# Kernel optimization log

Hardware: AMD Instinct MI355X
Metric: run time of the kernel (lower is better)

The kernel has to match this reference:

```python
import jax, jax.numpy as jnp
import numpy as np

EMBED_DIM = 1024
N_HEADS = 16
HEAD_DIM = EMBED_DIM // N_HEADS


def setup_inputs() -> dict:
    key = jax.random.key(0)
    k1, k2, k3 = jax.random.split(key, 3)
    B, T, C = 2, 2048, EMBED_DIM
    x = jax.random.normal(k1, (B, T, C), dtype=jnp.float32)
    # nn.Linear-style init scale
    s = 1.0 / np.sqrt(C)
    Wqkv = jax.random.normal(k2, (C, 3 * C), dtype=jnp.float32) * s
    bqkv = jnp.zeros((3 * C,), dtype=jnp.float32)
    Wout = jax.random.normal(k3, (C, C), dtype=jnp.float32) * s
    bout = jnp.zeros((C,), dtype=jnp.float32)
    return {"x": x, "Wqkv": Wqkv, "bqkv": bqkv, "Wout": Wout, "bout": bout}


def reference(x, Wqkv, bqkv, Wout, bout):
    B, T, C = x.shape
    H, D = N_HEADS, HEAD_DIM
    qkv = x @ Wqkv + bqkv  # [B,T,3C]
    q, k, v = jnp.split(qkv, 3, axis=-1)
    # [B,T,C] -> [B,H,T,D]
    q = q.reshape(B, T, H, D).transpose(0, 2, 1, 3)
    k = k.reshape(B, T, H, D).transpose(0, 2, 1, 3)
    v = v.reshape(B, T, H, D).transpose(0, 2, 1, 3)
    scale = 1.0 / np.sqrt(D)
    scores = jnp.einsum("bhqd,bhkd->bhqk", q, k) * scale  # [B,H,T,T]
    causal = jnp.tril(jnp.ones((T, T), dtype=bool))  # True where allowed
    scores = jnp.where(causal, scores, jnp.finfo(scores.dtype).min)
    attn = jax.nn.softmax(scores, axis=-1)
    out = jnp.einsum("bhqk,bhkd->bhqd", attn, v)  # [B,H,T,D]
    out = out.transpose(0, 2, 1, 3).reshape(B, T, C)
    return out @ Wout + bout
```

## Files before the change

### kernel.cpp

```cpp
#include <hip/hip_runtime.h>
#include <hip/hip_bf16.h>
#include <stdint.h>

#define EMBED 1024
#define NH 16
#define HD 64
#define BATCH 2
#define SEQ 2048
#define MTOK (BATCH*SEQ)

using bf8 = __attribute__((ext_vector_type(8))) short;
using f4  = __attribute__((ext_vector_type(4))) float;
using f16v = __attribute__((ext_vector_type(16))) float;
using u16x4 = __attribute__((ext_vector_type(4))) unsigned short;

union U4 { uint32_t u[4]; bf8 v; };

__device__ __forceinline__ uint32_t pk_bf16(float a, float b) {
  __hip_bfloat162 h = __float22bfloat162_rn(float2{a, b});
  union { __hip_bfloat162 h; uint32_t u; } c; c.h = h; return c.u;
}
__device__ __forceinline__ unsigned short bfbits(float f) {
  __hip_bfloat16 h = __float2bfloat16(f);
  union { __hip_bfloat16 h; unsigned short u; } c; c.h = h; return c.u;
}
__device__ __forceinline__ float bf2f(unsigned short u) {
  union { uint32_t u; float f; } c; c.u = (uint32_t)u << 16; return c.f;
}
__device__ __forceinline__ float fexp2(float x) {
#if __has_builtin(__builtin_amdgcn_exp2f)
  return __builtin_amdgcn_exp2f(x);
#else
  return exp2f(x);
#endif
}
__device__ __forceinline__ float frcp(float x) {
#if __has_builtin(__builtin_amdgcn_rcpf)
  return __builtin_amdgcn_rcpf(x);
#else
  return 1.f / x;
#endif
}

__device__ __forceinline__ void gl2lds16(const void* g, void* l) {
  __builtin_amdgcn_global_load_lds(
      (const __attribute__((address_space(1))) void*)g,
      (__attribute__((address_space(3))) void*)l, 16, 0, 0);
}

__global__ __launch_bounds__(256) void prep(const float* __restrict__ x,
                                            unsigned short* __restrict__ xb,
                                            const float* __restrict__ Wqkv,
                                            unsigned short* __restrict__ wqkvT,
                                            const float* __restrict__ Wout,
                                            unsigned short* __restrict__ woutT) {
  __shared__ float tl[64][65];
  int blk = blockIdx.x;
  if (blk < 4096) {
    int i = (blk * 256 + threadIdx.x) * 4;
    float4 v = *(const float4*)(x + i);
    uint2 o;
    o.x = pk_bf16(v.x, v.y);
    o.y = pk_bf16(v.z, v.w);
    *(uint2*)(xb + i) = o;
    return;
  }
  const float* W; unsigned short* Wt; int K, N, bx, by;
  if (blk < 4096 + 768) {
    int j = blk - 4096; W = Wqkv; Wt = wqkvT; K = 1024; N = 3072;
    bx = j % 48; by = j / 48;
  } else {
    int j = blk - 4096 - 768; W = Wout; Wt = woutT; K = 1024; N = 1024;
    bx = j % 16; by = j / 16;
  }
  int k0 = by * 64, n0 = bx * 64;
  int tr = threadIdx.x >> 6, tc = threadIdx.x & 63;
#pragma unroll
  for (int i = 0; i < 16; i++) {
    int r = tr + i * 4;
    tl[r][tc] = W[(size_t)(k0 + r) * N + n0 + tc];
  }
  __syncthreads();
#pragma unroll
  for (int i = 0; i < 16; i++) {
    int r = tr + i * 4;
    Wt[(size_t)(n0 + r) * K + k0 + tc] = bfbits(tl[tc][r]);
  }
}

template<int BN, int MODE>
__global__ __launch_bounds__(256) void gemm_bt(const unsigned short* __restrict__ A,
                                               const unsigned short* __restrict__ Bt,
                                               const float* __restrict__ bias,
                                               unsigned short* __restrict__ Oq,
                                               unsigned short* __restrict__ Ov,
                                               float* __restrict__ Of,
                                               int M, int N, int K) {
  constexpr int MT = (BN == 128) ? 4 : 2;
  const int tid = threadIdx.x;
  const int w = tid >> 6, lane = tid & 63;
  const int wm = (BN == 128) ? (w >> 1) : w;
  const int wn = (BN == 128) ? (w & 1) : 0;
  const int m0 = blockIdx.y * 128, n0 = blockIdx.x * BN;

  __shared__ char smem[16384 + BN * 128];
  char* Al = smem;
  char* Bl = smem + 16384;

  f4 acc[MT][4] = {};

  for (int k0 = 0; k0 < K; k0 += 64) {
    __syncthreads();
#pragma unroll
    for (int i = 0; i < 4; i++) {
      int row = w * 8 + i * 32 + (lane >> 3);
      int col = ((lane & 7) * 8) ^ ((row & 7) << 3);
      gl2lds16(A + (size_t)(m0 + row) * K + k0 + col, Al + (w * 8 + i * 32) * 128);
    }
#pragma unroll
    for (int i = 0; i < BN / 32; i++) {
      int row = w * 8 + i * 32 + (lane >> 3);
      int col = ((lane & 7) * 8) ^ ((row & 7) << 3);
      gl2lds16(Bt + (size_t)(n0 + row) * K + k0 + col, Bl + (w * 8 + i * 32) * 128);
    }
    __syncthreads();
#pragma unroll
    for (int ks = 0; ks < 2; ks++) {
      bf8 af[MT], bfr[4];
#pragma unroll
      for (int mt = 0; mt < MT; mt++) {
        int rr = wm * (MT * 16) + mt * 16 + (lane & 15);
        af[mt] = *(const bf8*)(Al + rr * 128 + ((ks * 64 + (lane >> 4) * 16) ^ ((rr & 7) << 4)));
      }
#pragma unroll
      for (int nt = 0; nt < 4; nt++) {
        int rr = wn * 64 + nt * 16 + (lane & 15);
        bfr[nt] = *(const bf8*)(Bl + rr * 128 + ((ks * 64 + (lane >> 4) * 16) ^ ((rr & 7) << 4)));
      }
#pragma unroll
      for (int mt = 0; mt < MT; mt++)
#pragma unroll
        for (int nt = 0; nt < 4; nt++)
          acc[mt][nt] = __builtin_amdgcn_mfma_f32_16x16x32_bf16(af[mt], bfr[nt], acc[mt][nt], 0, 0, 0);
    }
  }

  if (MODE == 0) {
#pragma unroll
    for (int nt = 0; nt < 4; nt++) {
      int n = n0 + wn * 64 + nt * 16 + (lane & 15);
      float bv = bias[n];
      int region = n >> 10, c = n & 1023, h = c >> 6, d = c & 63;
      float sc = (region == 0) ? 0.180336880f : 1.0f;
#pragma unroll
      for (int mt = 0; mt < MT; mt++) {
#pragma unroll
        for (int r = 0; r < 4; r++) {
          int m = m0 + wm * (MT * 16) + mt * 16 + (lane >> 4) * 4 + r;
          int b = m >> 11, t = m & 2047;
          unsigned short val = bfbits((acc[mt][nt][r] + bv) * sc);
          if (region < 2) {
            size_t off = ((((size_t)region * 2 + b) * 16 + h) * 2048 + t) * 64 + d;
            Oq[off] = val;
          } else {
            size_t off = (((size_t)b * 16 + h) * 64 + d) * 2048 + t;
            Ov[off] = val;
          }
        }
      }
    }
  } else {
#pragma unroll
    for (int mt = 0; mt < MT; mt++) {
#pragma unroll
      for (int r = 0; r < 4; r++) {
        int m = m0 + wm * (MT * 16) + mt * 16 + (lane >> 4) * 4 + r;
#pragma unroll
        for (int nt = 0; nt < 4; nt++) {
          int n = n0 + wn * 64 + nt * 16 + (lane & 15);
          Of[(size_t)m * N + n] = acc[mt][nt][r] + bias[n];
        }
      }
    }
  }
}

__global__ __launch_bounds__(256) void attn9(const unsigned short* __restrict__ Qb,
                                             const unsigned short* __restrict__ Kb,
                                             const unsigned short* __restrict__ Vtb,
                                             unsigned short* __restrict__ Ob,
                                             unsigned short* __restrict__ partO,
                                             float* __restrict__ Lbuf) {
  const int idx = blockIdx.x;
  int qt, ts, te;
  const int bh = idx & 31;
  if (idx < 256)        { qt = 8 + (idx >> 5);          ts = 0;  te = 16; }
  else if (idx < 512)   { qt = 8 + ((idx - 256) >> 5);  ts = 16; te = 2 * qt + 2; }
  else                  { qt = 7 - ((idx - 512) >> 5);  ts = 0;  te = 2 * qt + 2; }

  const int tid = threadIdx.x;
  const int w = tid >> 6, lane = tid & 63;
  const int hi = lane >> 5, q32 = lane & 31;

  __shared__ char smem[32768];

  const unsigned short* Qg  = Qb  + (size_t)bh * SEQ * HD;
  const unsigned short* Kg  = Kb  + (size_t)bh * SEQ * HD;
  const unsigned short* Vtg = Vtb + (size_t)bh * SEQ * HD;

  const int qbw  = qt * 128 + w * 32;
  const int qrow = qbw + q32;

  bf8 qf[4];
#pragma unroll
  for (int kc = 0; kc < 4; kc++)
    qf[kc] = *(const bf8*)(Qg + (size_t)qrow * HD + kc * 16 + hi * 8);

  U4 ones;
#pragma unroll
  for (int i = 0; i < 4; i++) ones.u[i] = 0x3F803F80u;

  f16v acc0 = {}, acc1 = {}, accl = {};

  auto STAGE = [&](int buf, int t) {
    int kv0 = t * 64;
#pragma unroll
    for (int i = 0; i < 2; i++) {
      int c = i * 4 + w;
      int row = c * 8 + (lane >> 3);
      int col = ((lane & 7) * 8) ^ ((row & 7) << 3);
      gl2lds16(Kg + (size_t)(kv0 + row) * HD + col,    smem + buf * 8192 + c * 1024);
      gl2lds16(Vtg + (size_t)row * SEQ + kv0 + col,    smem + 16384 + buf * 8192 + c * 1024);
    }
  };

  const int nt_loc = te - ts;
  STAGE(0, ts);
  if (nt_loc > 1) STAGE(1, ts + 1);

  for (int tl = 0; tl < nt_loc; tl++) {
    const int t = ts + tl;
    const int kv0 = t * 64;

    if (tl + 1 < nt_loc) {
      asm volatile("s_waitcnt vmcnt(4)" ::: "memory");
    } else {
      asm volatile("s_waitcnt vmcnt(0)" ::: "memory");
    }
    __builtin_amdgcn_s_barrier();

    if (kv0 <= qbw + 31) {
      const char* kl = smem + (tl & 1) * 8192;
      const char* vl = smem + 16384 + (tl & 1) * 8192;
      const bool hi_vis = (kv0 + 32 <= qbw + 31);

      f16v s0 = {}, s1 = {};
      __builtin_amdgcn_s_setprio(1);
#pragma unroll
      for (int kc = 0; kc < 4; kc++) {
        int r0 = q32;
        bf8 k0 = *(const bf8*)(kl + r0 * 128 + ((kc * 32 + hi * 16) ^ ((r0 & 7) << 4)));
        s0 = __builtin_amdgcn_mfma_f32_32x32x16_bf16(k0, qf[kc], s0, 0, 0, 0);
      }
      if (hi_vis) {
#pragma unroll
        for (int kc = 0; kc < 4; kc++) {
          int r1 = 32 + q32;
          bf8 k1 = *(const bf8*)(kl + r1 * 128 + ((kc * 32 + hi * 16) ^ ((r1 & 7) << 4)));
          s1 = __builtin_amdgcn_mfma_f32_32x32x16_bf16(k1, qf[kc], s1, 0, 0, 0);
        }
      }
      __builtin_amdgcn_s_setprio(0);

      if (kv0 + 63 > qbw) {
#pragma unroll
        for (int r = 0; r < 16; r++) {
          int key = kv0 + (r & 3) + 8 * (r >> 2) + 4 * hi;
          if (key > qrow)      s0[r] = -1e30f;
          if (key + 32 > qrow) s1[r] = -1e30f;
        }
      }

      uint32_t u[16];
#pragma unroll
      for (int m8 = 0; m8 < 8; m8++) {
        float pa = fexp2(s0[2 * m8]), pb = fexp2(s0[2 * m8 + 1]);
        u[m8] = pk_bf16(pa, pb);
      }
      if (hi_vis) {
#pragma unroll
        for (int m8 = 0; m8 < 8; m8++) {
          float pc = fexp2(s1[2 * m8]), pd = fexp2(s1[2 * m8 + 1]);
          u[8 + m8] = pk_bf16(pc, pd);
        }
      }

      __builtin_amdgcn_s_setprio(1);
      const int ncc = hi_vis ? 4 : 2;
      for (int kcc = 0; kcc < ncc; kcc++) {
        const int base = (kcc >> 1) * 8 + (kcc & 1) * 4;
        uint32_t a0 = u[base + 0], a2 = u[base + 2];
        uint32_t a1 = u[base + 1], a3 = u[base + 3];
        asm("v_permlane32_swap_b32 %0, %1" : "+v"(a0), "+v"(a2));
        asm("v_permlane32_swap_b32 %0, %1" : "+v"(a1), "+v"(a3));
        U4 f; f.u[0] = a0; f.u[1] = a1; f.u[2] = a2; f.u[3] = a3;
        int r0 = q32, r1 = 32 + q32;
        bf8 v0 = *(const bf8*)(vl + r0 * 128 + ((kcc * 32 + hi * 16) ^ ((r0 & 7) << 4)));
        bf8 v1 = *(const bf8*)(vl + r1 * 128 + ((kcc * 32 + hi * 16) ^ ((r1 & 7) << 4)));
        acc0 = __builtin_amdgcn_mfma_f32_32x32x16_bf16(f.v, v0, acc0, 0, 0, 0);
        acc1 = __builtin_amdgcn_mfma_f32_32x32x16_bf16(f.v, v1, acc1, 0, 0, 0);
        accl = __builtin_amdgcn_mfma_f32_32x32x16_bf16(f.v, ones.v, accl, 0, 0, 0);
      }
      __builtin_amdgcn_s_setprio(0);
    }

    __builtin_amdgcn_s_barrier();
    if (tl + 2 < nt_loc) STAGE(tl & 1, t + 2);
  }

  if (qt < 8) {
    int b = bh >> 4, h = bh & 15;
    unsigned short* Og = Ob + (size_t)b * SEQ * EMBED;
#pragma unroll
    for (int r = 0; r < 16; r++) {
      int ql_ = (r & 3) + 8 * (r >> 2) + 4 * hi;
      float linv = frcp(accl[r]);
      size_t rowoff = (size_t)(qbw + ql_) * EMBED + h * 64;
      Og[rowoff + q32]      = bfbits(acc0[r] * linv);
      Og[rowoff + 32 + q32] = bfbits(acc1[r] * linv);
    }
  } else {
    int seg = (ts == 16) ? 1 : 0;
    int part = ((qt - 8) * 32 + bh) * 2 + seg;
    unsigned short* P0 = partO + (size_t)part * 8192;
#pragma unroll
    for (int r = 0; r < 16; r++) {
      int ql_ = (r & 3) + 8 * (r >> 2) + 4 * hi;
      int rowl = w * 32 + ql_;
      P0[rowl * 64 + q32]      = bfbits(acc0[r]);
      P0[rowl * 64 + 32 + q32] = bfbits(acc1[r]);
    }
    if (q32 == 0) {
#pragma unroll
      for (int r = 0; r < 16; r++) {
        int ql_ = (r & 3) + 8 * (r >> 2) + 4 * hi;
        Lbuf[part * 128 + w * 32 + ql_] = accl[r];
      }
    }
  }
}

__global__ __launch_bounds__(256) void attn_combine(const unsigned short* __restrict__ partO,
                                                    const float* __restrict__ Lbuf,
                                                    unsigned short* __restrict__ Ob) {
  int pair = blockIdx.x;
  int qt = 8 + (pair >> 5), bh = pair & 31;
  int p0 = pair * 2, p1 = p0 + 1;
  int b = bh >> 4, h = bh & 15;
#pragma unroll
  for (int rr = 0; rr < 2; rr++) {
    int row = rr * 64 + (threadIdx.x >> 2);
    int d0 = (threadIdx.x & 3) * 16;
    float l0 = Lbuf[p0 * 128 + row], l1 = Lbuf[p1 * 128 + row];
    float linv = 1.f / (l0 + l1);
    const unsigned short* O0 = partO + (size_t)p0 * 8192 + row * 64 + d0;
    const unsigned short* O1 = partO + (size_t)p1 * 8192 + row * 64 + d0;
    unsigned short* out = Ob + ((size_t)b * SEQ + qt * 128 + row) * EMBED + h * 64 + d0;
    u16x4 res[4];
#pragma unroll
    for (int v = 0; v < 4; v++) {
      u16x4 a = *(const u16x4*)(O0 + v * 4);
      u16x4 c = *(const u16x4*)(O1 + v * 4);
#pragma unroll
      for (int e = 0; e < 4; e++)
        res[v][e] = bfbits(linv * (bf2f(a[e]) + bf2f(c[e])));
    }
    *(u16x4*)(out)      = res[0];
    *(u16x4*)(out + 4)  = res[1];
    *(u16x4*)(out + 8)  = res[2];
    *(u16x4*)(out + 12) = res[3];
  }
}

extern "C" void kernel_launch(void* const* d_in, const int* in_sizes, int n_in,
                              void* d_out, int out_size, void* d_ws, size_t ws_size,
                              hipStream_t stream) {
  const float* x    = (const float*)d_in[0];
  const float* Wqkv = (const float*)d_in[1];
  const float* bqkv = (const float*)d_in[2];
  const float* Wout = (const float*)d_in[3];
  const float* bout = (const float*)d_in[4];
  float* out = (float*)d_out;

  char* ws = (char*)d_ws;
  unsigned short* xb    = (unsigned short*)ws;
  unsigned short* partO = (unsigned short*)ws;
  unsigned short* wqkvT = (unsigned short*)(ws + (size_t)8  * 1048576);
  float*          lbuf  = (float*)(ws + (size_t)8 * 1048576);
  unsigned short* woutT = (unsigned short*)(ws + (size_t)14 * 1048576);
  unsigned short* qk    = (unsigned short*)(ws + (size_t)16 * 1048576);
  unsigned short* vT    = (unsigned short*)(ws + (size_t)32 * 1048576);
  unsigned short* obuf  = (unsigned short*)(ws + (size_t)40 * 1048576);

  prep<<<dim3(4096 + 768 + 256), 256, 0, stream>>>(x, xb, Wqkv, wqkvT, Wout, woutT);

  gemm_bt<128, 0><<<dim3(24, 32), 256, 0, stream>>>(xb, wqkvT, bqkv, qk, vT, nullptr,
                                                    MTOK, 3 * EMBED, EMBED);

  const unsigned short* Qb = qk;
  const unsigned short* Kb = qk + (size_t)BATCH * NH * SEQ * HD;
  attn9<<<dim3(768), 256, 0, stream>>>(Qb, Kb, vT, obuf, partO, lbuf);
  attn_combine<<<dim3(256), 256, 0, stream>>>(partO, lbuf, obuf);

  gemm_bt<64, 1><<<dim3(16, 32), 256, 0, stream>>>(obuf, woutT, bout, nullptr, nullptr, out,
                                                   MTOK, EMBED, EMBED);
}
```

Measured before the change: 114.3 us.

## Rebalance causal attention work with table-driven splits of at most eleven KV tiles

Replaces the fixed two-way KV split for the upper half of query tiles with a table-driven schedule. Every block now processes at most 11 KV tiles, long query tiles are split into two or three segments, and blocks are ordered longest first. The combine kernel handles a variable number of partials for query tiles 5 to 15. The aim is to reduce tail imbalance across the causal workload, at the cost of more blocks, more partial writes and a larger combine pass.

```diff
diff --git a/kernel.cpp b/kernel.cpp
--- a/kernel.cpp
+++ b/kernel.cpp
@@ -185,18 +185,21 @@
   }
 }
 
-__global__ __launch_bounds__(256) void attn9(const unsigned short* __restrict__ Qb,
-                                             const unsigned short* __restrict__ Kb,
-                                             const unsigned short* __restrict__ Vtb,
-                                             unsigned short* __restrict__ Ob,
-                                             unsigned short* __restrict__ partO,
-                                             float* __restrict__ Lbuf) {
+__global__ __launch_bounds__(256) void attn11(const unsigned short* __restrict__ Qb,
+                                              const unsigned short* __restrict__ Kb,
+                                              const unsigned short* __restrict__ Vtb,
+                                              unsigned short* __restrict__ Ob,
+                                              unsigned short* __restrict__ partO,
+                                              float* __restrict__ Lbuf) {
+  static const signed char QTs[32] = {15,15,14,14,13,13,12,12,11,11,10,10,9,8,7,6,5,15,4,9,14,3,8,13,2,7,12,1,6,11,0,5};
+  static const signed char TSs[32] = {0,11,0,11,0,11,0,11,0,11,0,11,0,0,0,0,0,22,0,11,22,0,11,22,0,11,22,0,11,22,0,11};
+  static const signed char PS[32]  = {0,1,2,3,4,5,6,7,8,9,10,11,12,13,14,15,16,17,-1,18,19,-1,20,21,-1,22,23,-1,24,25,-1,26};
   const int idx = blockIdx.x;
-  int qt, ts, te;
-  const int bh = idx & 31;
-  if (idx < 256)        { qt = 8 + (idx >> 5);          ts = 0;  te = 16; }
-  else if (idx < 512)   { qt = 8 + ((idx - 256) >> 5);  ts = 16; te = 2 * qt + 2; }
-  else                  { qt = 7 - ((idx - 512) >> 5);  ts = 0;  te = 2 * qt + 2; }
+  const int s = idx >> 5, bh = idx & 31;
+  const int qt = QTs[s], ts = TSs[s];
+  const int ntot = 2 * qt + 2;
+  const int te = min(ts + 11, ntot);
+  const int slot = PS[s];
 
   const int tid = threadIdx.x;
   const int w = tid >> 6, lane = tid & 63;
@@ -318,7 +321,7 @@
     if (tl + 2 < nt_loc) STAGE(tl & 1, t + 2);
   }
 
-  if (qt < 8) {
+  if (slot < 0) {
     int b = bh >> 4, h = bh & 15;
     unsigned short* Og = Ob + (size_t)b * SEQ * EMBED;
 #pragma unroll
@@ -330,9 +333,8 @@
       Og[rowoff + 32 + q32] = bfbits(acc1[r] * linv);
     }
   } else {
-    int seg = (ts == 16) ? 1 : 0;
-    int part = ((qt - 8) * 32 + bh) * 2 + seg;
-    unsigned short* P0 = partO + (size_t)part * 8192;
+    int pidx = slot * 32 + bh;
+    unsigned short* P0 = partO + (size_t)pidx * 8192;
 #pragma unroll
     for (int r = 0; r < 16; r++) {
       int ql_ = (r & 3) + 8 * (r >> 2) + 4 * hi;
@@ -344,7 +346,7 @@
 #pragma unroll
       for (int r = 0; r < 16; r++) {
         int ql_ = (r & 3) + 8 * (r >> 2) + 4 * hi;
-        Lbuf[part * 128 + w * 32 + ql_] = accl[r];
+        Lbuf[pidx * 128 + w * 32 + ql_] = accl[r];
       }
     }
   }
@@ -353,27 +355,39 @@
 __global__ __launch_bounds__(256) void attn_combine(const unsigned short* __restrict__ partO,
                                                     const float* __restrict__ Lbuf,
                                                     unsigned short* __restrict__ Ob) {
+  static const signed char NSg[11] = {2,2,2,2,2,2,3,3,3,3,3};
+  static const signed char SL[11][3] = {
+    {16,26,0},{15,24,0},{14,22,0},{13,20,0},{12,18,0},{10,11,0},
+    {8,9,25},{6,7,23},{4,5,21},{2,3,19},{0,1,17}};
   int pair = blockIdx.x;
-  int qt = 8 + (pair >> 5), bh = pair & 31;
-  int p0 = pair * 2, p1 = p0 + 1;
+  int qi = pair >> 5, bh = pair & 31;
+  int qt = 5 + qi;
+  int ns = NSg[qi];
   int b = bh >> 4, h = bh & 15;
 #pragma unroll
   for (int rr = 0; rr < 2; rr++) {
     int row = rr * 64 + (threadIdx.x >> 2);
     int d0 = (threadIdx.x & 3) * 16;
-    float l0 = Lbuf[p0 * 128 + row], l1 = Lbuf[p1 * 128 + row];
-    float linv = 1.f / (l0 + l1);
-    const unsigned short* O0 = partO + (size_t)p0 * 8192 + row * 64 + d0;
-    const unsigned short* O1 = partO + (size_t)p1 * 8192 + row * 64 + d0;
+    float lsum = 0.f;
+    float acc[16] = {};
+    for (int sg = 0; sg < ns; sg++) {
+      int pidx = (int)SL[qi][sg] * 32 + bh;
+      lsum += Lbuf[pidx * 128 + row];
+      const unsigned short* O0 = partO + (size_t)pidx * 8192 + row * 64 + d0;
+#pragma unroll
+      for (int v = 0; v < 4; v++) {
+        u16x4 a = *(const u16x4*)(O0 + v * 4);
+#pragma unroll
+        for (int e = 0; e < 4; e++) acc[v * 4 + e] += bf2f(a[e]);
+      }
+    }
+    float linv = 1.f / lsum;
     unsigned short* out = Ob + ((size_t)b * SEQ + qt * 128 + row) * EMBED + h * 64 + d0;
     u16x4 res[4];
 #pragma unroll
     for (int v = 0; v < 4; v++) {
-      u16x4 a = *(const u16x4*)(O0 + v * 4);
-      u16x4 c = *(const u16x4*)(O1 + v * 4);
-#pragma unroll
-      for (int e = 0; e < 4; e++)
-        res[v][e] = bfbits(linv * (bf2f(a[e]) + bf2f(c[e])));
+#pragma unroll
+      for (int e = 0; e < 4; e++) res[v][e] = bfbits(acc[v * 4 + e] * linv);
     }
     *(u16x4*)(out)      = res[0];
     *(u16x4*)(out + 4)  = res[1];
@@ -394,9 +408,9 @@
 
   char* ws = (char*)d_ws;
   unsigned short* xb    = (unsigned short*)ws;
+  unsigned short* wqkvT = (unsigned short*)(ws + (size_t)8 * 1048576);
   unsigned short* partO = (unsigned short*)ws;
-  unsigned short* wqkvT = (unsigned short*)(ws + (size_t)8  * 1048576);
-  float*          lbuf  = (float*)(ws + (size_t)8 * 1048576);
+  float*          lbuf  = (float*)(ws + 14155776);
   unsigned short* woutT = (unsigned short*)(ws + (size_t)14 * 1048576);
   unsigned short* qk    = (unsigned short*)(ws + (size_t)16 * 1048576);
   unsigned short* vT    = (unsigned short*)(ws + (size_t)32 * 1048576);
@@ -409,8 +423,8 @@
 
   const unsigned short* Qb = qk;
   const unsigned short* Kb = qk + (size_t)BATCH * NH * SEQ * HD;
-  attn9<<<dim3(768), 256, 0, stream>>>(Qb, Kb, vT, obuf, partO, lbuf);
-  attn_combine<<<dim3(256), 256, 0, stream>>>(partO, lbuf, obuf);
+  attn11<<<dim3(32 * 32), 256, 0, stream>>>(Qb, Kb, vT, obuf, partO, lbuf);
+  attn_combine<<<dim3(11 * 32), 256, 0, stream>>>(partO, lbuf, obuf);
 
   gemm_bt<64, 1><<<dim3(16, 32), 256, 0, stream>>>(obuf, woutT, bout, nullptr, nullptr, out,
                                                    MTOK, EMBED, EMBED);
```

Measured after the change: 116.6 us. 1.02x slower.
